# Optimization experiments

Measured on AMD Instinct MI355X. Metric: run time of the kernel, lower is better.

Reference implementation:

```python
import jax, jax.numpy as jnp
import numpy as np

B, LENGTH, D, IN = 32, 32, 384, 384
NCELLS = LENGTH * (LENGTH + 1) // 2  # 528

def _offsets():
    off = np.zeros(LENGTH, dtype=np.int64)
    for lvl in range(1, LENGTH):
        off[lvl] = off[lvl - 1] + (LENGTH - (lvl - 1))
    return off

_OFF = _offsets()

def _inside_index(level):
    Ls = LENGTH - level
    pos = np.arange(Ls)[:, None]
    k = np.arange(level)[None, :]
    left = _OFF[k] + pos                      # span (k, pos)
    right = _OFF[level - k - 1] + pos + k + 1  # span (level-k-1, pos+k+1)
    return jnp.asarray(left), jnp.asarray(right)

def _outside_index(level):
    Ls = LENGTH - level
    N = LENGTH - level - 1  # constant #contexts per position
    par = np.zeros((Ls, N), dtype=np.int64)
    sib = np.zeros((Ls, N), dtype=np.int64)
    for pos in range(Ls):
        j = 0
        for s in range(LENGTH - pos - level - 1):  # node is left child
            par[pos, j] = _OFF[level + s + 1] + pos
            sib[pos, j] = _OFF[s] + pos + level + 1
            j += 1
        for s in range(pos):  # node is right child
            par[pos, j] = _OFF[level + s + 1] + pos - s - 1
            sib[pos, j] = _OFF[s] + pos - s - 1
            j += 1
    return jnp.asarray(par), jnp.asarray(sib)

def sigma_h(x):
    return x * jnp.tanh(jnp.sqrt(jax.nn.sigmoid(x)))

def layer_norm(x, g, b, eps=1e-5):
    mu = x.mean(-1, keepdims=True)
    var = ((x - mu) ** 2).mean(-1, keepdims=True)
    return (x - mu) * jax.lax.rsqrt(var + eps) * g + b

def compose(l, r, W0, W1, B0, W2, B1):
    h = sigma_h(l @ W0 + r @ W1 + B0)
    return sigma_h(h @ W2 + B1)

def bilinear(u, v, M):
    return jnp.einsum('blnd,de,blne->bln', u, M, v)[..., None]

def setup_inputs() -> dict:
    key = jax.random.key(0)
    ks = jax.random.split(key, 16)
    sc = 1.0 / np.sqrt(D)
    mk = lambda k, shp: (jax.random.normal(k, shp, dtype=jnp.float32) * sc)
    inp = {
        'x': jax.random.normal(ks[0], (B, LENGTH, IN), dtype=jnp.float32),
        'leaf_W': mk(ks[1], (IN, D)), 'leaf_b': jnp.zeros((D,), jnp.float32),
        'in_ln_g': jnp.ones((D,), jnp.float32), 'in_ln_b': jnp.zeros((D,), jnp.float32),
        'out_ln_g': jnp.ones((D,), jnp.float32), 'out_ln_b': jnp.zeros((D,), jnp.float32),
        'root_h': jax.random.normal(ks[2], (D,), dtype=jnp.float32) * 0.02,
        'in_bi': mk(ks[3], (D, D)), 'out_bi': mk(ks[4], (D, D)),
        'in_W0': mk(ks[5], (D, D)), 'in_W1': mk(ks[6], (D, D)),
        'in_B0': jnp.zeros((D,), jnp.float32),
        'in_W2': mk(ks[7], (D, D)), 'in_B1': jnp.zeros((D,), jnp.float32),
        'out_W0': mk(ks[8], (D, D)), 'out_W1': mk(ks[9], (D, D)),
        'out_B0': jnp.zeros((D,), jnp.float32),
        'out_W2': mk(ks[10], (D, D)), 'out_B1': jnp.zeros((D,), jnp.float32),
    }
    return inp

def reference(x, leaf_W, leaf_b, in_ln_g, in_ln_b, out_ln_g, out_ln_b, root_h,
              in_bi, out_bi, in_W0, in_W1, in_B0, in_W2, in_B1,
              out_W0, out_W1, out_B0, out_W2, out_B1):
    # leaf transform
    h0 = layer_norm(sigma_h(x @ leaf_W + leaf_b), in_ln_g, in_ln_b)
    ih = jnp.zeros((B, NCELLS, D), x.dtype).at[:, :LENGTH].set(h0)
    is_ = jnp.zeros((B, NCELLS, 1), x.dtype)
    # inside pass (CKY chart, level-by-level)
    for level in range(1, LENGTH):
        li, ri = _inside_index(level)
        lh, rh = ih[:, li], ih[:, ri]   # [B, Ls, level, D]
        ls, rs = is_[:, li], is_[:, ri]
        sc = bilinear(lh, rh, in_bi) + ls + rs
        p = jax.nn.softmax(sc, axis=2)
        xc = compose(lh, rh, in_W0, in_W1, in_B0, in_W2, in_B1)
        hbar = layer_norm((p * xc).sum(2), in_ln_g, in_ln_b)
        sbar = (p * sc).sum(2)
        o = int(_OFF[level]); Ls = LENGTH - level
        ih = ih.at[:, o:o + Ls].set(hbar)
        is_ = is_.at[:, o:o + Ls].set(sbar)
    # outside pass
    oh = jnp.zeros((B, NCELLS, D), x.dtype)
    os_ = jnp.zeros((B, NCELLS, 1), x.dtype)
    root = layer_norm(jnp.broadcast_to(root_h, (B, 1, D)), out_ln_g, out_ln_b)
    oh = oh.at[:, -1:].set(root)
    for level in range(LENGTH - 2, -1, -1):
        pi, si = _outside_index(level)
        ph, sh = oh[:, pi], ih[:, si]   # parent outside / sibling inside
        ps, ss = os_[:, pi], is_[:, si]
        sc = bilinear(sh, ph, out_bi) + ss + ps
        p = jax.nn.softmax(sc, axis=2)
        xc = compose(ph, sh, out_W0, out_W1, out_B0, out_W2, out_B1)
        hbar = layer_norm((p * xc).sum(2), out_ln_g, out_ln_b)
        sbar = (p * sc).sum(2)
        o = int(_OFF[level]); Ls = LENGTH - level
        oh = oh.at[:, o:o + Ls].set(hbar)
        os_ = os_.at[:, o:o + Ls].set(sbar)
    return ih, is_, oh, os_
```

## Files before the change

kernel.cpp:

```cpp
#include <hip/hip_runtime.h>
#include <cstddef>

#define BDIM 32
#define LEN 32
#define DD 384
#define NCELLS 528

typedef _Float16 h16;
typedef __attribute__((ext_vector_type(8))) _Float16 v8h;
typedef __attribute__((ext_vector_type(4))) float v4f;

__device__ __forceinline__ int offf(int k) { return k * 32 - ((k * (k - 1)) >> 1); }
static inline int offh(int k) { return k * 32 - ((k * (k - 1)) >> 1); }

__device__ __forceinline__ float sigma_h_f(float x) {
  float s = 1.0f / (1.0f + __expf(-x));
  float r = sqrtf(s);
  float e2 = __expf(2.0f * r);
  float th = 1.0f - 2.0f / (e2 + 1.0f);
  return x * th;
}

__device__ __forceinline__ size_t rowbase(int r, int gLs, int gOff) {
  if (gLs == 0) return (size_t)r;
  int b = r / gLs;
  int p = r - b * gLs;
  return (size_t)b * NCELLS + gOff + p;
}

__device__ __forceinline__ void split16(float v, h16& h, h16& l) {
  h = (h16)v;
  l = (h16)(v - (float)h);
}

__global__ __launch_bounds__(256) void pack3_k(
    const float* __restrict__ w0, const float* __restrict__ w1,
    const float* __restrict__ bi, const float* __restrict__ ow1,
    const float* __restrict__ obi, const float* __restrict__ w2,
    const float* __restrict__ ow2, const float* __restrict__ ow0,
    const float* __restrict__ lw, const float* __restrict__ x,
    h16* __restrict__ WCth, h16* __restrict__ WCtl,
    h16* __restrict__ W2th, h16* __restrict__ W2tl,
    h16* __restrict__ OW2th, h16* __restrict__ OW2tl,
    h16* __restrict__ OW0th, h16* __restrict__ OW0tl,
    h16* __restrict__ LWth, h16* __restrict__ LWtl,
    h16* __restrict__ xh, h16* __restrict__ xl,
    float* __restrict__ isp, float* __restrict__ osp) {
  int i = blockIdx.x * 256 + threadIdx.x;
  if (i < 1920 * 384) {
    int n = i / 384, k = i - n * 384;
    int sel = n / 384, c = n - sel * 384;
    const float* src = sel == 0 ? w0 : sel == 1 ? w1 : sel == 2 ? bi
                       : sel == 3 ? ow1 : obi;
    float v = src[k * 384 + c];
    h16 h, l; split16(v, h, l);
    WCth[i] = h; WCtl[i] = l;
  }
  if (i < 384 * 384) {
    int n = i / 384, k = i - n * 384;
    h16 h, l;
    split16(w2[k * 384 + n], h, l);  W2th[i] = h;  W2tl[i] = l;
    split16(ow2[k * 384 + n], h, l); OW2th[i] = h; OW2tl[i] = l;
    split16(ow0[k * 384 + n], h, l); OW0th[i] = h; OW0tl[i] = l;
    split16(lw[k * 384 + n], h, l);  LWth[i] = h;  LWtl[i] = l;
  }
  if (i < 1024 * 384) {
    h16 h, l; split16(x[i], h, l);
    xh[i] = h; xl[i] = l;
  }
  if (i < BDIM * NCELLS) { isp[i] = 0.0f; osp[i] = 0.0f; }
}

__global__ __launch_bounds__(256) void gemmh(
    const h16* __restrict__ Ahp, const h16* __restrict__ Alp,
    const h16* __restrict__ Bth, const h16* __restrict__ Btl,
    const float* __restrict__ bias, float* __restrict__ C,
    int M, int N, int act, int gLs, int gOff) {
  __shared__ h16 Ah[64][40], Al[64][40];
  __shared__ h16 Bh[128][40], Bl[128][40];
  int tid = threadIdx.x;
  int w = tid >> 6, lane = tid & 63;

  int nbx = gridDim.x, nby = gridDim.y;
  int total = nbx * nby;
  int lin = blockIdx.y * nbx + blockIdx.x;
  int xcd = lin & 7, slot = lin >> 3;
  int qd = total >> 3, rd = total & 7;
  int wk = (xcd < rd ? xcd * (qd + 1) : rd * (qd + 1) + (xcd - rd) * qd) + slot;
  int bx = wk / nby;
  int by = wk - bx * nby;
  int m0 = bx * 64, n0 = by * 128;
  int r = lane & 15, q = lane >> 4;

  v4f acc[4][2];
#pragma unroll
  for (int i = 0; i < 4; ++i)
#pragma unroll
    for (int j = 0; j < 2; ++j) acc[i][j] = (v4f){0.f, 0.f, 0.f, 0.f};

  int sar = tid >> 2;
  int sak = (tid & 3) << 3;
  const h16* Aph = nullptr;
  const h16* Apl = nullptr;
  if (m0 + sar < M) {
    size_t rb = (size_t)(m0 + sar) * DD;
    Aph = Ahp + rb + sak;
    Apl = Alp + rb + sak;
  }
  int sbc = tid >> 1;
  int sbk = (tid & 1) << 4;
  const h16* Bph = Bth + (size_t)(n0 + sbc) * DD + sbk;
  const h16* Bpl = Btl + (size_t)(n0 + sbc) * DD + sbk;

  for (int k0 = 0; k0 < DD; k0 += 32) {
    v8h a_h = (v8h){0.f, 0.f, 0.f, 0.f, 0.f, 0.f, 0.f, 0.f};
    v8h a_l = a_h;
    if (Aph) {
      a_h = *reinterpret_cast<const v8h*>(Aph + k0);
      a_l = *reinterpret_cast<const v8h*>(Apl + k0);
    }
    v8h b_h0 = *reinterpret_cast<const v8h*>(Bph + k0);
    v8h b_h1 = *reinterpret_cast<const v8h*>(Bph + k0 + 8);
    v8h b_l0 = *reinterpret_cast<const v8h*>(Bpl + k0);
    v8h b_l1 = *reinterpret_cast<const v8h*>(Bpl + k0 + 8);
    __syncthreads();
    *reinterpret_cast<v8h*>(&Ah[sar][sak]) = a_h;
    *reinterpret_cast<v8h*>(&Al[sar][sak]) = a_l;
    *reinterpret_cast<v8h*>(&Bh[sbc][sbk]) = b_h0;
    *reinterpret_cast<v8h*>(&Bh[sbc][sbk + 8]) = b_h1;
    *reinterpret_cast<v8h*>(&Bl[sbc][sbk]) = b_l0;
    *reinterpret_cast<v8h*>(&Bl[sbc][sbk + 8]) = b_l1;
    __syncthreads();
    v8h afh[4], afl[4], bfh[2], bfl[2];
#pragma unroll
    for (int i = 0; i < 4; ++i) {
      afh[i] = *reinterpret_cast<const v8h*>(&Ah[i * 16 + r][q * 8]);
      afl[i] = *reinterpret_cast<const v8h*>(&Al[i * 16 + r][q * 8]);
    }
#pragma unroll
    for (int j = 0; j < 2; ++j) {
      bfh[j] = *reinterpret_cast<const v8h*>(&Bh[w * 32 + j * 16 + r][q * 8]);
      bfl[j] = *reinterpret_cast<const v8h*>(&Bl[w * 32 + j * 16 + r][q * 8]);
    }
#pragma unroll
    for (int i = 0; i < 4; ++i)
#pragma unroll
      for (int j = 0; j < 2; ++j) {
        acc[i][j] = __builtin_amdgcn_mfma_f32_16x16x32_f16(afl[i], bfh[j], acc[i][j], 0, 0, 0);
        acc[i][j] = __builtin_amdgcn_mfma_f32_16x16x32_f16(afh[i], bfl[j], acc[i][j], 0, 0, 0);
        acc[i][j] = __builtin_amdgcn_mfma_f32_16x16x32_f16(afh[i], bfh[j], acc[i][j], 0, 0, 0);
      }
  }

#pragma unroll
  for (int i = 0; i < 4; ++i) {
#pragma unroll
    for (int reg = 0; reg < 4; ++reg) {
      int rr = m0 + i * 16 + q * 4 + reg;
      if (rr >= M) continue;
      size_t cb = rowbase(rr, gLs, gOff) * (size_t)N;
#pragma unroll
      for (int j = 0; j < 2; ++j) {
        int col = n0 + w * 32 + j * 16 + r;
        float v = acc[i][j][reg];
        if (bias) v += bias[col];
        if (act) v = sigma_h_f(v);
        C[cb + col] = v;
      }
    }
  }
}

__global__ __launch_bounds__(256) void k1_in(
    const float* __restrict__ PC, const float* __restrict__ ihp,
    float* __restrict__ isp, h16* __restrict__ Hh, h16* __restrict__ Hl,
    float* __restrict__ Pw, const float* __restrict__ B0,
    int L, int Ls, int offL) {
  int g = blockIdx.x;
  int b = g / Ls, pos = g - b * Ls;
  int tid = threadIdx.x, lane = tid & 63, wv = tid >> 6;
  __shared__ float scs[32];
  __shared__ float b0s[384];
  size_t cb = (size_t)b * NCELLS;
  for (int k = tid; k < 384; k += 256) b0s[k] = B0[k];
  __syncthreads();
  for (int n = wv; n < L; n += 4) {
    int lc = offf(n) + pos;
    int rc = offf(L - 1 - n) + pos + n + 1;
    const float* u = PC + (cb + lc) * 1920 + 768;
    const float* v = ihp + (cb + rc) * (size_t)DD;
    float s = 0.0f;
#pragma unroll
    for (int jj = 0; jj < 6; ++jj) s += u[lane + 64 * jj] * v[lane + 64 * jj];
#pragma unroll
    for (int o = 32; o; o >>= 1) s += __shfl_xor(s, o, 64);
    if (lane == 0) scs[n] = s + isp[cb + lc] + isp[cb + rc];
    const float* A0r = PC + (cb + lc) * 1920;
    const float* A1r = PC + (cb + rc) * 1920 + 384;
    size_t hb = ((size_t)g * L + n) * DD;
#pragma unroll
    for (int jj = 0; jj < 6; ++jj) {
      int k = lane + 64 * jj;
      float hv = sigma_h_f(A0r[k] + A1r[k] + b0s[k]);
      h16 h = (h16)hv;
      Hh[hb + k] = h;
      Hl[hb + k] = (h16)(hv - (float)h);
    }
  }
  __syncthreads();
  if (wv == 0) {
    float v = (lane < L) ? scs[lane] : -3.0e38f;
    float m = v;
#pragma unroll
    for (int o = 32; o; o >>= 1) m = fmaxf(m, __shfl_xor(m, o, 64));
    float e = (lane < L) ? __expf(v - m) : 0.0f;
    float S = e;
#pragma unroll
    for (int o = 32; o; o >>= 1) S += __shfl_xor(S, o, 64);
    float pn = e / S;
    if (lane < L) Pw[(size_t)g * L + lane] = pn;
    float sb = (lane < L) ? pn * v : 0.0f;
#pragma unroll
    for (int o = 32; o; o >>= 1) sb += __shfl_xor(sb, o, 64);
    if (lane == 0) isp[cb + offL + pos] = sb;
  }
}

__global__ __launch_bounds__(256) void k1_out(
    const float* __restrict__ PC, const float* __restrict__ P0,
    const float* __restrict__ ohp, const float* __restrict__ isp,
    float* __restrict__ osp, h16* __restrict__ Hh, h16* __restrict__ Hl,
    float* __restrict__ Pw, const float* __restrict__ B0,
    int L, int Ls, int Nc, int offL) {
  int g = blockIdx.x;
  int b = g / Ls, pos = g - b * Ls;
  int tid = threadIdx.x, lane = tid & 63, wv = tid >> 6;
  __shared__ float scs[32];
  __shared__ float b0s[384];
  size_t cb = (size_t)b * NCELLS;
  int cnt0 = 31 - pos - L;
  for (int k = tid; k < 384; k += 256) b0s[k] = B0[k];
  __syncthreads();
  for (int j = wv; j < Nc; j += 4) {
    int par, sib;
    if (j < cnt0) { par = offf(L + j + 1) + pos; sib = offf(j) + pos + L + 1; }
    else { int s2 = j - cnt0; par = offf(L + s2 + 1) + pos - s2 - 1; sib = offf(s2) + pos - s2 - 1; }
    const float* u = PC + (cb + sib) * 1920 + 1536;
    const float* v = ohp + (cb + par) * (size_t)DD;
    float s = 0.0f;
#pragma unroll
    for (int jj = 0; jj < 6; ++jj) s += u[lane + 64 * jj] * v[lane + 64 * jj];
#pragma unroll
    for (int o = 32; o; o >>= 1) s += __shfl_xor(s, o, 64);
    if (lane == 0) scs[j] = s + isp[cb + sib] + osp[cb + par];
    const float* p0r = P0 + (cb + par) * (size_t)DD;
    const float* s1r = PC + (cb + sib) * 1920 + 1152;
    size_t hb = ((size_t)g * Nc + j) * DD;
#pragma unroll
    for (int jj = 0; jj < 6; ++jj) {
      int k = lane + 64 * jj;
      float hv = sigma_h_f(p0r[k] + s1r[k] + b0s[k]);
      h16 h = (h16)hv;
      Hh[hb + k] = h;
      Hl[hb + k] = (h16)(hv - (float)h);
    }
  }
  __syncthreads();
  if (wv == 0) {
    float v = (lane < Nc) ? scs[lane] : -3.0e38f;
    float m = v;
#pragma unroll
    for (int o = 32; o; o >>= 1) m = fmaxf(m, __shfl_xor(m, o, 64));
    float e = (lane < Nc) ? __expf(v - m) : 0.0f;
    float S = e;
#pragma unroll
    for (int o = 32; o; o >>= 1) S += __shfl_xor(S, o, 64);
    float pn = e / S;
    if (lane < Nc) Pw[(size_t)g * Nc + lane] = pn;
    float sb = (lane < Nc) ? pn * v : 0.0f;
#pragma unroll
    for (int o = 32; o; o >>= 1) sb += __shfl_xor(sb, o, 64);
    if (lane == 0) osp[cb + offL + pos] = sb;
  }
}

__global__ __launch_bounds__(128) void k3_red_ln(
    const float* __restrict__ XC, const float* __restrict__ Pw,
    const float* __restrict__ lng, const float* __restrict__ lnb,
    float* __restrict__ outArr, h16* __restrict__ outh, h16* __restrict__ outl,
    int L, int Ls, int offL) {
  int g = blockIdx.x;
  int b = g / Ls, pos = g - b * Ls;
  int tid = threadIdx.x;
  float a0 = 0, a1 = 0, a2 = 0;
  const float* base = XC + (size_t)g * L * DD;
  for (int n = 0; n < L; ++n) {
    float pw = Pw ? Pw[(size_t)g * L + n] : 1.0f;
    const float* row = base + (size_t)n * DD;
    a0 += pw * row[tid];
    a1 += pw * row[tid + 128];
    a2 += pw * row[tid + 256];
  }
  int lane = tid & 63, wv = tid >> 6;
  float s = a0 + a1 + a2;
#pragma unroll
  for (int o = 32; o; o >>= 1) s += __shfl_xor(s, o, 64);
  __shared__ float r1[2], r2[2];
  if (lane == 0) r1[wv] = s;
  __syncthreads();
  float mean = (r1[0] + r1[1]) * (1.0f / 384.0f);
  float d0 = a0 - mean, d1 = a1 - mean, d2 = a2 - mean;
  float q = d0 * d0 + d1 * d1 + d2 * d2;
#pragma unroll
  for (int o = 32; o; o >>= 1) q += __shfl_xor(q, o, 64);
  if (lane == 0) r2[wv] = q;
  __syncthreads();
  float var = (r2[0] + r2[1]) * (1.0f / 384.0f);
  float inv = rsqrtf(var + 1e-5f);
  size_t ob = ((size_t)b * NCELLS + offL + pos) * DD;
  float* out = outArr + ob;
  float v0 = d0 * inv * lng[tid]       + lnb[tid];
  float v1 = d1 * inv * lng[tid + 128] + lnb[tid + 128];
  float v2 = d2 * inv * lng[tid + 256] + lnb[tid + 256];
  out[tid]       = v0;
  out[tid + 128] = v1;
  out[tid + 256] = v2;
  size_t sb = (size_t)g * DD;
  h16 h;
  h = (h16)v0; outh[sb + tid]       = h; outl[sb + tid]       = (h16)(v0 - (float)h);
  h = (h16)v1; outh[sb + tid + 128] = h; outl[sb + tid + 128] = (h16)(v1 - (float)h);
  h = (h16)v2; outh[sb + tid + 256] = h; outl[sb + tid + 256] = (h16)(v2 - (float)h);
}

__global__ __launch_bounds__(384) void root_k(
    const float* __restrict__ rooth, const float* __restrict__ lng,
    const float* __restrict__ lnb, const float* __restrict__ W0,
    float* __restrict__ ohp, float* __restrict__ P0) {
  int tid = threadIdx.x;
  int lane = tid & 63, wv = tid >> 6;
  __shared__ float rl[384];
  __shared__ float r1[6], r2[6];
  float x = rooth[tid];
  float s = x;
#pragma unroll
  for (int o = 32; o; o >>= 1) s += __shfl_xor(s, o, 64);
  if (lane == 0) r1[wv] = s;
  __syncthreads();
  float mean = (r1[0] + r1[1] + r1[2] + r1[3] + r1[4] + r1[5]) * (1.0f / 384.0f);
  float d = x - mean;
  float q = d * d;
#pragma unroll
  for (int o = 32; o; o >>= 1) q += __shfl_xor(q, o, 64);
  if (lane == 0) r2[wv] = q;
  __syncthreads();
  float var = (r2[0] + r2[1] + r2[2] + r2[3] + r2[4] + r2[5]) * (1.0f / 384.0f);
  float inv = rsqrtf(var + 1e-5f);
  float v = d * inv * lng[tid] + lnb[tid];
  rl[tid] = v;
  __syncthreads();
  for (int b2 = 0; b2 < BDIM; ++b2)
    ohp[((size_t)b2 * NCELLS + 527) * DD + tid] = v;
  float acc = 0.0f;
  for (int d2 = 0; d2 < 384; ++d2) acc += rl[d2] * W0[(size_t)d2 * 384 + tid];
  for (int b2 = 0; b2 < BDIM; ++b2)
    P0[((size_t)b2 * NCELLS + 527) * DD + tid] = acc;
}

extern "C" void kernel_launch(void* const* d_in, const int* in_sizes, int n_in,
                              void* d_out, int out_size, void* d_ws, size_t ws_size,
                              hipStream_t stream) {
  const float* x        = (const float*)d_in[0];
  const float* leaf_W   = (const float*)d_in[1];
  const float* leaf_b   = (const float*)d_in[2];
  const float* in_ln_g  = (const float*)d_in[3];
  const float* in_ln_b  = (const float*)d_in[4];
  const float* out_ln_g = (const float*)d_in[5];
  const float* out_ln_b = (const float*)d_in[6];
  const float* root_h   = (const float*)d_in[7];
  const float* in_bi    = (const float*)d_in[8];
  const float* out_bi   = (const float*)d_in[9];
  const float* in_W0    = (const float*)d_in[10];
  const float* in_W1    = (const float*)d_in[11];
  const float* in_B0    = (const float*)d_in[12];
  const float* in_W2    = (const float*)d_in[13];
  const float* in_B1    = (const float*)d_in[14];
  const float* out_W0   = (const float*)d_in[15];
  const float* out_W1   = (const float*)d_in[16];
  const float* out_B0   = (const float*)d_in[17];
  const float* out_W2   = (const float*)d_in[18];
  const float* out_B1   = (const float*)d_in[19];

  float* ih  = (float*)d_out;
  float* isp = ih + (size_t)BDIM * NCELLS * DD;
  float* oh  = isp + (size_t)BDIM * NCELLS;
  float* osp = oh + (size_t)BDIM * NCELLS * DD;

  float* PC  = (float*)d_ws;
  float* P0  = PC + (size_t)32440320;
  float* XCb = P0 + (size_t)6488064;
  float* Pw  = XCb + (size_t)12189696;
  h16* Hh    = (h16*)(Pw + 31744);
  h16* Hl    = Hh + (size_t)12189696;
  h16* WCth  = Hl + (size_t)12189696;
  h16* WCtl  = WCth + (size_t)737280;
  h16* W2th  = WCtl + (size_t)737280;
  h16* W2tl  = W2th + (size_t)147456;
  h16* OW2th = W2tl + (size_t)147456;
  h16* OW2tl = OW2th + (size_t)147456;
  h16* OW0th = OW2tl + (size_t)147456;
  h16* OW0tl = OW0th + (size_t)147456;
  h16* LWth  = OW0tl + (size_t)147456;
  h16* LWtl  = LWth + (size_t)147456;
  h16* xh = Hh;
  h16* xl = Hl;
  h16* Ch = Hh + (size_t)16384 * DD;
  h16* Cl = Hl + (size_t)16384 * DD;

  pack3_k<<<2880, 256, 0, stream>>>(in_W0, in_W1, in_bi, out_W1, out_bi,
                                    in_W2, out_W2, out_W0, leaf_W, x,
                                    WCth, WCtl, W2th, W2tl, OW2th, OW2tl,
                                    OW0th, OW0tl, LWth, LWtl, xh, xl,
                                    isp, osp);

  gemmh<<<dim3(16, 3), 256, 0, stream>>>(xh, xl, LWth, LWtl, leaf_b, XCb, 1024, 384, 1, 0, 0);
  k3_red_ln<<<1024, 128, 0, stream>>>(XCb, nullptr, in_ln_g, in_ln_b, ih, Ch, Cl, 1, 32, 0);
  gemmh<<<dim3(16, 15), 256, 0, stream>>>(Ch, Cl, WCth, WCtl, nullptr, PC, 1024, 1920, 0, 32, 0);

  for (int L = 1; L < LEN; ++L) {
    int Ls = LEN - L, G = BDIM * Ls, M = G * L, off = offh(L);
    k1_in<<<G, 256, 0, stream>>>(PC, ih, isp, Hh, Hl, Pw, in_B0, L, Ls, off);
    gemmh<<<dim3((M + 63) / 64, 3), 256, 0, stream>>>(Hh, Hl, W2th, W2tl, in_B1, XCb, M, 384, 1, 0, 0);
    k3_red_ln<<<G, 128, 0, stream>>>(XCb, Pw, in_ln_g, in_ln_b, ih, Ch, Cl, L, Ls, off);
    gemmh<<<dim3((G + 63) / 64, 15), 256, 0, stream>>>(Ch, Cl, WCth, WCtl, nullptr, PC, G, 1920, 0, Ls, off);
  }

  root_k<<<1, 384, 0, stream>>>(root_h, out_ln_g, out_ln_b, out_W0, oh, P0);

  for (int L = LEN - 2; L >= 0; --L) {
    int Ls = LEN - L, G = BDIM * Ls, Nc = LEN - 1 - L, M = G * Nc, off = offh(L);
    k1_out<<<G, 256, 0, stream>>>(PC, P0, oh, isp, osp, Hh, Hl, Pw, out_B0, L, Ls, Nc, off);
    gemmh<<<dim3((M + 63) / 64, 3), 256, 0, stream>>>(Hh, Hl, OW2th, OW2tl, out_B1, XCb, M, 384, 1, 0, 0);
    k3_red_ln<<<G, 128, 0, stream>>>(XCb, Pw, out_ln_g, out_ln_b, oh, Ch, Cl, Nc, Ls, off);
    if (L > 0)
      gemmh<<<dim3((G + 63) / 64, 3), 256, 0, stream>>>(Ch, Cl, OW0th, OW0tl, nullptr, P0, G, 384, 0, Ls, off);
  }
}
```

Before: 4.851 ms.

## Split per-cell child work across more blocks and move softmax into reduction

The score/hidden kernel now launches a second grid dimension over child pairs, so each block handles up to four children instead of looping over all of them. The softmax over children moves into the weighted-reduction/layernorm kernel, which now uses 256 threads split into two halves that each reduce half the rows. Inside and outside variants are unified into shared kernels. The aim is more parallelism on the long serial chain of small levels, at the cost of recomputing index bias in the reduction kernel and one extra final gemm launch.

```diff
diff --git a/kernel.cpp b/kernel.cpp
--- a/kernel.cpp
+++ b/kernel.cpp
@@ -171,165 +171,149 @@
   }
 }
 
-__global__ __launch_bounds__(256) void k1_in(
-    const float* __restrict__ PC, const float* __restrict__ ihp,
-    float* __restrict__ isp, h16* __restrict__ Hh, h16* __restrict__ Hl,
-    float* __restrict__ Pw, const float* __restrict__ B0,
-    int L, int Ls, int offL) {
+__global__ __launch_bounds__(256) void k1s(
+    const float* __restrict__ PC, const float* __restrict__ P0,
+    const float* __restrict__ vArr, float* __restrict__ scores,
+    h16* __restrict__ Hh, h16* __restrict__ Hl,
+    const float* __restrict__ B0, int lvl, int np, int Ls, int inside) {
   int g = blockIdx.x;
   int b = g / Ls, pos = g - b * Ls;
   int tid = threadIdx.x, lane = tid & 63, wv = tid >> 6;
-  __shared__ float scs[32];
   __shared__ float b0s[384];
   size_t cb = (size_t)b * NCELLS;
   for (int k = tid; k < 384; k += 256) b0s[k] = B0[k];
   __syncthreads();
-  for (int n = wv; n < L; n += 4) {
+  int n = blockIdx.y * 4 + wv;
+  if (n >= np) return;
+
+  const float *u, *v, *A0r, *A1r;
+  if (inside) {
     int lc = offf(n) + pos;
-    int rc = offf(L - 1 - n) + pos + n + 1;
-    const float* u = PC + (cb + lc) * 1920 + 768;
-    const float* v = ihp + (cb + rc) * (size_t)DD;
-    float s = 0.0f;
-#pragma unroll
-    for (int jj = 0; jj < 6; ++jj) s += u[lane + 64 * jj] * v[lane + 64 * jj];
-#pragma unroll
-    for (int o = 32; o; o >>= 1) s += __shfl_xor(s, o, 64);
-    if (lane == 0) scs[n] = s + isp[cb + lc] + isp[cb + rc];
-    const float* A0r = PC + (cb + lc) * 1920;
-    const float* A1r = PC + (cb + rc) * 1920 + 384;
-    size_t hb = ((size_t)g * L + n) * DD;
-#pragma unroll
-    for (int jj = 0; jj < 6; ++jj) {
-      int k = lane + 64 * jj;
-      float hv = sigma_h_f(A0r[k] + A1r[k] + b0s[k]);
-      h16 h = (h16)hv;
-      Hh[hb + k] = h;
-      Hl[hb + k] = (h16)(hv - (float)h);
-    }
-  }
-  __syncthreads();
-  if (wv == 0) {
-    float v = (lane < L) ? scs[lane] : -3.0e38f;
-    float m = v;
-#pragma unroll
-    for (int o = 32; o; o >>= 1) m = fmaxf(m, __shfl_xor(m, o, 64));
-    float e = (lane < L) ? __expf(v - m) : 0.0f;
-    float S = e;
-#pragma unroll
-    for (int o = 32; o; o >>= 1) S += __shfl_xor(S, o, 64);
-    float pn = e / S;
-    if (lane < L) Pw[(size_t)g * L + lane] = pn;
-    float sb = (lane < L) ? pn * v : 0.0f;
-#pragma unroll
-    for (int o = 32; o; o >>= 1) sb += __shfl_xor(sb, o, 64);
-    if (lane == 0) isp[cb + offL + pos] = sb;
-  }
-}
-
-__global__ __launch_bounds__(256) void k1_out(
-    const float* __restrict__ PC, const float* __restrict__ P0,
-    const float* __restrict__ ohp, const float* __restrict__ isp,
-    float* __restrict__ osp, h16* __restrict__ Hh, h16* __restrict__ Hl,
-    float* __restrict__ Pw, const float* __restrict__ B0,
-    int L, int Ls, int Nc, int offL) {
+    int rc = offf(np - 1 - n) + pos + n + 1;
+    u   = PC + (cb + lc) * 1920 + 768;
+    v   = vArr + (cb + rc) * (size_t)DD;
+    A0r = PC + (cb + lc) * 1920;
+    A1r = PC + (cb + rc) * 1920 + 384;
+  } else {
+    int par, sib;
+    int cnt0 = 31 - pos - lvl;
+    if (n < cnt0) { par = offf(lvl + n + 1) + pos; sib = offf(n) + pos + lvl + 1; }
+    else { int s2 = n - cnt0; par = offf(lvl + s2 + 1) + pos - s2 - 1; sib = offf(s2) + pos - s2 - 1; }
+    u   = PC + (cb + sib) * 1920 + 1536;
+    v   = vArr + (cb + par) * (size_t)DD;
+    A0r = P0 + (cb + par) * (size_t)DD;
+    A1r = PC + (cb + sib) * 1920 + 1152;
+  }
+  float s = 0.0f;
+#pragma unroll
+  for (int jj = 0; jj < 6; ++jj) s += u[lane + 64 * jj] * v[lane + 64 * jj];
+#pragma unroll
+  for (int o = 32; o; o >>= 1) s += __shfl_xor(s, o, 64);
+  if (lane == 0) scores[(size_t)g * np + n] = s;
+  size_t hb = ((size_t)g * np + n) * DD;
+#pragma unroll
+  for (int jj = 0; jj < 6; ++jj) {
+    int k = lane + 64 * jj;
+    float hv = sigma_h_f(A0r[k] + A1r[k] + b0s[k]);
+    h16 h = (h16)hv;
+    Hh[hb + k] = h;
+    Hl[hb + k] = (h16)(hv - (float)h);
+  }
+}
+
+__global__ __launch_bounds__(256) void k3_sm(
+    const float* __restrict__ XC, const float* __restrict__ scores,
+    const float* __restrict__ isp, float* __restrict__ sOut,
+    const float* __restrict__ lng, const float* __restrict__ lnb,
+    float* __restrict__ outArr, h16* __restrict__ outh, h16* __restrict__ outl,
+    int lvl, int np, int Ls, int offL, int inside, int doSM) {
   int g = blockIdx.x;
   int b = g / Ls, pos = g - b * Ls;
   int tid = threadIdx.x, lane = tid & 63, wv = tid >> 6;
-  __shared__ float scs[32];
-  __shared__ float b0s[384];
+  __shared__ float pb[32];
+  __shared__ float comb[384];
+  __shared__ float r1[2], r2[2];
   size_t cb = (size_t)b * NCELLS;
-  int cnt0 = 31 - pos - L;
-  for (int k = tid; k < 384; k += 256) b0s[k] = B0[k];
-  __syncthreads();
-  for (int j = wv; j < Nc; j += 4) {
-    int par, sib;
-    if (j < cnt0) { par = offf(L + j + 1) + pos; sib = offf(j) + pos + L + 1; }
-    else { int s2 = j - cnt0; par = offf(L + s2 + 1) + pos - s2 - 1; sib = offf(s2) + pos - s2 - 1; }
-    const float* u = PC + (cb + sib) * 1920 + 1536;
-    const float* v = ohp + (cb + par) * (size_t)DD;
-    float s = 0.0f;
-#pragma unroll
-    for (int jj = 0; jj < 6; ++jj) s += u[lane + 64 * jj] * v[lane + 64 * jj];
-#pragma unroll
-    for (int o = 32; o; o >>= 1) s += __shfl_xor(s, o, 64);
-    if (lane == 0) scs[j] = s + isp[cb + sib] + osp[cb + par];
-    const float* p0r = P0 + (cb + par) * (size_t)DD;
-    const float* s1r = PC + (cb + sib) * 1920 + 1152;
-    size_t hb = ((size_t)g * Nc + j) * DD;
-#pragma unroll
-    for (int jj = 0; jj < 6; ++jj) {
-      int k = lane + 64 * jj;
-      float hv = sigma_h_f(p0r[k] + s1r[k] + b0s[k]);
-      h16 h = (h16)hv;
-      Hh[hb + k] = h;
-      Hl[hb + k] = (h16)(hv - (float)h);
+
+  if (doSM) {
+    if (wv == 0) {
+      float sc = -3.0e38f;
+      if (lane < np) {
+        float biasv;
+        if (inside) {
+          int lc = offf(lane) + pos;
+          int rc = offf(np - 1 - lane) + pos + lane + 1;
+          biasv = isp[cb + lc] + isp[cb + rc];
+        } else {
+          int par, sib;
+          int cnt0 = 31 - pos - lvl;
+          if (lane < cnt0) { par = offf(lvl + lane + 1) + pos; sib = offf(lane) + pos + lvl + 1; }
+          else { int s2 = lane - cnt0; par = offf(lvl + s2 + 1) + pos - s2 - 1; sib = offf(s2) + pos - s2 - 1; }
+          biasv = isp[cb + sib] + sOut[cb + par];
+        }
+        sc = scores[(size_t)g * np + lane] + biasv;
+      }
+      float m = sc;
+#pragma unroll
+      for (int o = 32; o; o >>= 1) m = fmaxf(m, __shfl_xor(m, o, 64));
+      float e = (lane < np) ? __expf(sc - m) : 0.0f;
+      float S = e;
+#pragma unroll
+      for (int o = 32; o; o >>= 1) S += __shfl_xor(S, o, 64);
+      float pn = e / S;
+      if (lane < np) pb[lane] = pn;
+      float sb = (lane < np) ? pn * sc : 0.0f;
+#pragma unroll
+      for (int o = 32; o; o >>= 1) sb += __shfl_xor(sb, o, 64);
+      if (lane == 0) sOut[cb + offL + pos] = sb;
     }
-  }
-  __syncthreads();
-  if (wv == 0) {
-    float v = (lane < Nc) ? scs[lane] : -3.0e38f;
-    float m = v;
-#pragma unroll
-    for (int o = 32; o; o >>= 1) m = fmaxf(m, __shfl_xor(m, o, 64));
-    float e = (lane < Nc) ? __expf(v - m) : 0.0f;
-    float S = e;
-#pragma unroll
-    for (int o = 32; o; o >>= 1) S += __shfl_xor(S, o, 64);
-    float pn = e / S;
-    if (lane < Nc) Pw[(size_t)g * Nc + lane] = pn;
-    float sb = (lane < Nc) ? pn * v : 0.0f;
-#pragma unroll
-    for (int o = 32; o; o >>= 1) sb += __shfl_xor(sb, o, 64);
-    if (lane == 0) osp[cb + offL + pos] = sb;
-  }
-}
-
-__global__ __launch_bounds__(128) void k3_red_ln(
-    const float* __restrict__ XC, const float* __restrict__ Pw,
-    const float* __restrict__ lng, const float* __restrict__ lnb,
-    float* __restrict__ outArr, h16* __restrict__ outh, h16* __restrict__ outl,
-    int L, int Ls, int offL) {
-  int g = blockIdx.x;
-  int b = g / Ls, pos = g - b * Ls;
-  int tid = threadIdx.x;
-  float a0 = 0, a1 = 0, a2 = 0;
-  const float* base = XC + (size_t)g * L * DD;
-  for (int n = 0; n < L; ++n) {
-    float pw = Pw ? Pw[(size_t)g * L + n] : 1.0f;
+  } else {
+    if (tid == 0) pb[0] = 1.0f;
+  }
+  __syncthreads();
+
+  int gi = tid >> 7, t2 = tid & 127;
+  float a0 = 0.f, a1 = 0.f, a2 = 0.f;
+  const float* base = XC + (size_t)g * np * DD;
+  for (int n = gi; n < np; n += 2) {
+    float pw = pb[n];
     const float* row = base + (size_t)n * DD;
-    a0 += pw * row[tid];
-    a1 += pw * row[tid + 128];
-    a2 += pw * row[tid + 256];
-  }
-  int lane = tid & 63, wv = tid >> 6;
+    a0 += pw * row[t2];
+    a1 += pw * row[t2 + 128];
+    a2 += pw * row[t2 + 256];
+  }
+  if (gi == 1) { comb[t2] = a0; comb[t2 + 128] = a1; comb[t2 + 256] = a2; }
+  __syncthreads();
+  if (gi == 0) { a0 += comb[t2]; a1 += comb[t2 + 128]; a2 += comb[t2 + 256]; }
   float s = a0 + a1 + a2;
 #pragma unroll
   for (int o = 32; o; o >>= 1) s += __shfl_xor(s, o, 64);
-  __shared__ float r1[2], r2[2];
-  if (lane == 0) r1[wv] = s;
+  if (gi == 0 && lane == 0) r1[wv] = s;
   __syncthreads();
   float mean = (r1[0] + r1[1]) * (1.0f / 384.0f);
   float d0 = a0 - mean, d1 = a1 - mean, d2 = a2 - mean;
   float q = d0 * d0 + d1 * d1 + d2 * d2;
 #pragma unroll
   for (int o = 32; o; o >>= 1) q += __shfl_xor(q, o, 64);
-  if (lane == 0) r2[wv] = q;
-  __syncthreads();
-  float var = (r2[0] + r2[1]) * (1.0f / 384.0f);
-  float inv = rsqrtf(var + 1e-5f);
-  size_t ob = ((size_t)b * NCELLS + offL + pos) * DD;
-  float* out = outArr + ob;
-  float v0 = d0 * inv * lng[tid]       + lnb[tid];
-  float v1 = d1 * inv * lng[tid + 128] + lnb[tid + 128];
-  float v2 = d2 * inv * lng[tid + 256] + lnb[tid + 256];
-  out[tid]       = v0;
-  out[tid + 128] = v1;
-  out[tid + 256] = v2;
-  size_t sb = (size_t)g * DD;
-  h16 h;
-  h = (h16)v0; outh[sb + tid]       = h; outl[sb + tid]       = (h16)(v0 - (float)h);
-  h = (h16)v1; outh[sb + tid + 128] = h; outl[sb + tid + 128] = (h16)(v1 - (float)h);
-  h = (h16)v2; outh[sb + tid + 256] = h; outl[sb + tid + 256] = (h16)(v2 - (float)h);
+  if (gi == 0 && lane == 0) r2[wv] = q;
+  __syncthreads();
+  if (gi == 0) {
+    float var = (r2[0] + r2[1]) * (1.0f / 384.0f);
+    float inv = rsqrtf(var + 1e-5f);
+    size_t ob = ((size_t)b * NCELLS + offL + pos) * DD;
+    float* out = outArr + ob;
+    float v0 = d0 * inv * lng[t2]       + lnb[t2];
+    float v1 = d1 * inv * lng[t2 + 128] + lnb[t2 + 128];
+    float v2 = d2 * inv * lng[t2 + 256] + lnb[t2 + 256];
+    out[t2]       = v0;
+    out[t2 + 128] = v1;
+    out[t2 + 256] = v2;
+    size_t sb = (size_t)g * DD;
+    h16 h;
+    h = (h16)v0; outh[sb + t2]       = h; outl[sb + t2]       = (h16)(v0 - (float)h);
+    h = (h16)v1; outh[sb + t2 + 128] = h; outl[sb + t2 + 128] = (h16)(v1 - (float)h);
+    h = (h16)v2; outh[sb + t2 + 256] = h; outl[sb + t2 + 256] = (h16)(v2 - (float)h);
+  }
 }
 
 __global__ __launch_bounds__(384) void root_k(
@@ -423,14 +407,17 @@
                                     isp, osp);
 
   gemmh<<<dim3(16, 3), 256, 0, stream>>>(xh, xl, LWth, LWtl, leaf_b, XCb, 1024, 384, 1, 0, 0);
-  k3_red_ln<<<1024, 128, 0, stream>>>(XCb, nullptr, in_ln_g, in_ln_b, ih, Ch, Cl, 1, 32, 0);
+  k3_sm<<<1024, 256, 0, stream>>>(XCb, Pw, isp, isp, in_ln_g, in_ln_b,
+                                  ih, Ch, Cl, 0, 1, 32, 0, 1, 0);
   gemmh<<<dim3(16, 15), 256, 0, stream>>>(Ch, Cl, WCth, WCtl, nullptr, PC, 1024, 1920, 0, 32, 0);
 
   for (int L = 1; L < LEN; ++L) {
     int Ls = LEN - L, G = BDIM * Ls, M = G * L, off = offh(L);
-    k1_in<<<G, 256, 0, stream>>>(PC, ih, isp, Hh, Hl, Pw, in_B0, L, Ls, off);
+    k1s<<<dim3(G, (L + 3) / 4), 256, 0, stream>>>(PC, nullptr, ih, Pw, Hh, Hl,
+                                                  in_B0, L, L, Ls, 1);
     gemmh<<<dim3((M + 63) / 64, 3), 256, 0, stream>>>(Hh, Hl, W2th, W2tl, in_B1, XCb, M, 384, 1, 0, 0);
-    k3_red_ln<<<G, 128, 0, stream>>>(XCb, Pw, in_ln_g, in_ln_b, ih, Ch, Cl, L, Ls, off);
+    k3_sm<<<G, 256, 0, stream>>>(XCb, Pw, isp, isp, in_ln_g, in_ln_b,
+                                 ih, Ch, Cl, L, L, Ls, off, 1, 1);
     gemmh<<<dim3((G + 63) / 64, 15), 256, 0, stream>>>(Ch, Cl, WCth, WCtl, nullptr, PC, G, 1920, 0, Ls, off);
   }
 
@@ -438,10 +425,11 @@
 
   for (int L = LEN - 2; L >= 0; --L) {
     int Ls = LEN - L, G = BDIM * Ls, Nc = LEN - 1 - L, M = G * Nc, off = offh(L);
-    k1_out<<<G, 256, 0, stream>>>(PC, P0, oh, isp, osp, Hh, Hl, Pw, out_B0, L, Ls, Nc, off);
+    k1s<<<dim3(G, (Nc + 3) / 4), 256, 0, stream>>>(PC, P0, oh, Pw, Hh, Hl,
+                                                   out_B0, L, Nc, Ls, 0);
     gemmh<<<dim3((M + 63) / 64, 3), 256, 0, stream>>>(Hh, Hl, OW2th, OW2tl, out_B1, XCb, M, 384, 1, 0, 0);
-    k3_red_ln<<<G, 128, 0, stream>>>(XCb, Pw, out_ln_g, out_ln_b, oh, Ch, Cl, Nc, Ls, off);
-    if (L > 0)
-      gemmh<<<dim3((G + 63) / 64, 3), 256, 0, stream>>>(Ch, Cl, OW0th, OW0tl, nullptr, P0, G, 384, 0, Ls, off);
-  }
-}
+    k3_sm<<<G, 256, 0, stream>>>(XCb, Pw, isp, osp, out_ln_g, out_ln_b,
+                                 oh, Ch, Cl, L, Nc, Ls, off, 0, 1);
+    gemmh<<<dim3((G + 63) / 64, 3), 256, 0, stream>>>(Ch, Cl, OW0th, OW0tl, nullptr, P0, G, 384, 0, Ls, off);
+  }
+}
```

Measured after the change: 4.135 ms. 14.8% less time.
